# Kernel optimization log

Hardware: AMD Instinct MI355X
Metric: run time of the kernel (lower is better)

## Reference

```python
import jax, jax.numpy as jnp
import numpy as np

D_MODEL = 1024
NUM_HEADS = 16
SEQ_LEN = 2048
BATCH = 2
THETA = 10000.0


def apply_rope(x, positions, theta=THETA):
    # x: [b, h, s, d]; positions: [s] int
    d = x.shape[-1]
    inv_freq = 1.0 / (theta ** (jnp.arange(0, d, 2, dtype=jnp.float32) / d))  # [d/2]
    ang = positions.astype(jnp.float32)[:, None] * inv_freq[None, :]  # [s, d/2]
    cos, sin = jnp.cos(ang), jnp.sin(ang)  # [s, d/2]
    x_even = x[..., 0::2]
    x_odd = x[..., 1::2]
    out_even = x_even * cos - x_odd * sin
    out_odd = x_even * sin + x_odd * cos
    # re-interleave pairs
    out = jnp.stack([out_even, out_odd], axis=-1).reshape(x.shape)
    return out


def setup_inputs() -> dict:
    key = jax.random.key(0)
    ks = jax.random.split(key, 5)
    scale = 1.0 / np.sqrt(D_MODEL)
    return {
        "in_features": jax.random.normal(ks[0], (BATCH, SEQ_LEN, D_MODEL), dtype=jnp.float32),
        "token_positions": jnp.arange(SEQ_LEN, dtype=jnp.int32),
        "q_w": jax.random.normal(ks[1], (D_MODEL, D_MODEL), dtype=jnp.float32) * scale,
        "k_w": jax.random.normal(ks[2], (D_MODEL, D_MODEL), dtype=jnp.float32) * scale,
        "v_w": jax.random.normal(ks[3], (D_MODEL, D_MODEL), dtype=jnp.float32) * scale,
        "o_w": jax.random.normal(ks[4], (D_MODEL, D_MODEL), dtype=jnp.float32) * scale,
    }


def reference(in_features, token_positions, q_w, k_w, v_w, o_w):
    b, s, _ = in_features.shape
    h = NUM_HEADS
    d_k = D_MODEL // h

    # Linear stores weights [out, in]: y = x @ W^T
    def proj(x, w):
        y = jnp.einsum('bsi,oi->bso', x, w)
        return y.reshape(b, s, h, d_k).transpose(0, 2, 1, 3)  # [b, h, s, d]

    q = apply_rope(proj(in_features, q_w), token_positions)
    k = apply_rope(proj(in_features, k_w), token_positions)
    v = proj(in_features, v_w)

    scores = jnp.einsum('bhqd,bhkd->bhqk', q, k) / jnp.sqrt(jnp.float32(d_k))
    causal = jnp.tril(jnp.ones((s, s), dtype=bool))
    scores = jnp.where(causal, scores, jnp.float32(-1e30))
    attn = jax.nn.softmax(scores, axis=-1)
    out = jnp.einsum('bhqk,bhkd->bhqd', attn, v)  # [b, h, s, d]
    out = out.transpose(0, 2, 1, 3).reshape(b, s, h * d_k)
    return jnp.einsum('bsi,oi->bso', out, o_w)
```

## Files before the change

### kernel.cpp

```cpp
#include <hip/hip_runtime.h>
#include <hip/hip_bf16.h>

typedef unsigned short ushort_t;
typedef unsigned int uint_t;
typedef __attribute__((ext_vector_type(4))) float f32x4;
typedef __attribute__((ext_vector_type(16))) float f32x16;
typedef __attribute__((ext_vector_type(8))) short short8;
typedef __attribute__((ext_vector_type(4))) short short4x;
typedef __attribute__((ext_vector_type(4))) unsigned short u16x4;
typedef __attribute__((ext_vector_type(2))) uint_t u32x2;

typedef const __attribute__((address_space(1))) unsigned char glob_t;
typedef __attribute__((address_space(3))) unsigned char lds_t;

#define S_LEN 2048
#define DM 1024
#define NH 16
#define DH 64
#define NB 2
#define BH (NB*NH)
#define MROWS (NB*S_LEN)

#define SCALE_L2E 0.18033688f

__device__ __forceinline__ float bf2f(ushort_t u) {
    return __uint_as_float(((uint_t)u) << 16);
}
__device__ __forceinline__ ushort_t f2bf(float f) {
    __hip_bfloat16 h = __float2bfloat16(f);
    return *reinterpret_cast<ushort_t*>(&h);
}

__global__ __launch_bounds__(256) void convert_all(
    const float* __restrict__ X,  const float* __restrict__ Wq,
    const float* __restrict__ Wk, const float* __restrict__ Wv,
    const float* __restrict__ Wo,
    ushort_t* __restrict__ Xb,  ushort_t* __restrict__ Wqb,
    ushort_t* __restrict__ Wkb, ushort_t* __restrict__ Wvb,
    ushort_t* __restrict__ Wob)
{
    size_t i = (size_t)blockIdx.x * 256 + threadIdx.x;
    size_t e = i * 4;
    const float* src; ushort_t* dst; size_t off;
    if (e < (size_t)MROWS * DM) { src = X; dst = Xb; off = e; }
    else {
        size_t r = e - (size_t)MROWS * DM;
        int w = (int)(r >> 20); off = r & 1048575;
        src = (w == 0) ? Wq : (w == 1) ? Wk : (w == 2) ? Wv : Wo;
        dst = (w == 0) ? Wqb : (w == 1) ? Wkb : (w == 2) ? Wvb : Wob;
    }
    float4 v = *reinterpret_cast<const float4*>(src + off);
    u16x4 o;
    o[0] = f2bf(v.x); o[1] = f2bf(v.y); o[2] = f2bf(v.z); o[3] = f2bf(v.w);
    *reinterpret_cast<u16x4*>(dst + off) = o;
}

__global__ __launch_bounds__(256) void rope_table_k(
    const int* __restrict__ pos, float2* __restrict__ tab)
{
    int i = blockIdx.x * 256 + threadIdx.x;
    int s = i >> 5, f = i & 31;
    float inv = powf(10000.0f, -(float)f / 32.0f);
    float ang = (float)pos[s] * inv;
    tab[i] = make_float2(cosf(ang), sinf(ang));
}

template<int MODE>
__global__ __launch_bounds__(256) void gemm128b(
    const ushort_t* __restrict__ A,
    const ushort_t* __restrict__ W0, const ushort_t* __restrict__ W1,
    const ushort_t* __restrict__ W2,
    ushort_t* __restrict__ D0, ushort_t* __restrict__ D1,
    ushort_t* __restrict__ D2,
    float* __restrict__ Fout, const float2* __restrict__ tab)
{
    __shared__ __attribute__((aligned(16))) ushort_t As[128 * 32];
    __shared__ __attribute__((aligned(16))) ushort_t Bs[128 * 32];
    const ushort_t* W = (MODE == 1 || blockIdx.z == 0) ? W0
                        : (blockIdx.z == 1 ? W1 : W2);
    ushort_t* Dst = (blockIdx.z == 0) ? D0 : (blockIdx.z == 1) ? D1 : D2;
    int m0 = blockIdx.x * 128, n0 = blockIdx.y * 128;
    int tid = threadIdx.x, lane = tid & 63, wv = tid >> 6;
    int wm = wv >> 1, wn = wv & 1;
    int l15 = lane & 15, g = lane >> 4;

    f32x4 acc[4][4];
    for (int i = 0; i < 4; i++)
        for (int j = 0; j < 4; j++)
            acc[i][j] = (f32x4){0.f, 0.f, 0.f, 0.f};

    int srow = wv * 32 + (lane >> 2);
    int scol = (lane & 3) * 8;
    const ushort_t* Ap = A + (size_t)(m0 + srow) * DM + scol;
    const ushort_t* Wp = W + (size_t)(n0 + srow) * DM + scol;
    lds_t* laA0 = (lds_t*)&As[wv * 1024];
    lds_t* laA1 = (lds_t*)&As[wv * 1024 + 512];
    lds_t* laB0 = (lds_t*)&Bs[wv * 1024];
    lds_t* laB1 = (lds_t*)&Bs[wv * 1024 + 512];

    for (int kk = 0; kk < DM; kk += 32) {
        __builtin_amdgcn_global_load_lds((glob_t*)(Ap + kk), laA0, 16, 0, 0);
        __builtin_amdgcn_global_load_lds((glob_t*)(Ap + 16 * DM + kk), laA1, 16, 0, 0);
        __builtin_amdgcn_global_load_lds((glob_t*)(Wp + kk), laB0, 16, 0, 0);
        __builtin_amdgcn_global_load_lds((glob_t*)(Wp + 16 * DM + kk), laB1, 16, 0, 0);
        __syncthreads();
        short8 af[4], bf[4];
        for (int i = 0; i < 4; i++)
            af[i] = *reinterpret_cast<const short8*>(
                &As[(wm * 64 + i * 16 + l15) * 32 + g * 8]);
        for (int j = 0; j < 4; j++)
            bf[j] = *reinterpret_cast<const short8*>(
                &Bs[(wn * 64 + j * 16 + l15) * 32 + g * 8]);
        __builtin_amdgcn_s_setprio(1);
        for (int i = 0; i < 4; i++)
            for (int j = 0; j < 4; j++)
                acc[i][j] = __builtin_amdgcn_mfma_f32_16x16x32_bf16(
                    af[i], bf[j], acc[i][j], 0, 0, 0);
        __builtin_amdgcn_s_setprio(0);
        __syncthreads();
    }

    for (int i = 0; i < 4; i++) {
        for (int j = 0; j < 4; j++) {
            int mbase = m0 + wm * 64 + i * 16 + g * 4;
            int n = n0 + wn * 64 + j * 16 + l15;
            if (MODE == 0) {
                int h = n >> 6, d = n & 63;
                if (blockIdx.z < 2) {
                    int f = d >> 1;
                    float sgn = (d & 1) ? 1.f : -1.f;
                    float sc = (blockIdx.z == 0) ? SCALE_L2E : 1.0f;
                    for (int r = 0; r < 4; r++) {
                        int m = mbase + r;
                        int b = m >> 11, s = m & 2047;
                        float v = acc[i][j][r];
                        float p = __shfl_xor(v, 1);
                        float2 cs = tab[s * 32 + f];
                        float out = (v * cs.x + p * cs.y * sgn) * sc;
                        Dst[(((size_t)(b * NH + h)) * S_LEN + s) * DH + d] =
                            f2bf(out);
                    }
                } else {
                    for (int r = 0; r < 4; r++) {
                        int m = mbase + r;
                        int b = m >> 11, s = m & 2047;
                        Dst[((size_t)(b * NH + h) * DH + d) * S_LEN + s] =
                            f2bf(acc[i][j][r]);
                    }
                }
            } else {
                for (int r = 0; r < 4; r++)
                    Fout[(size_t)(mbase + r) * DM + n] = acc[i][j][r];
            }
        }
    }
}

#define WAITV4 asm volatile("s_waitcnt vmcnt(4)" ::: "memory")
#define WAITV0 asm volatile("s_waitcnt vmcnt(0)" ::: "memory")

__global__ __launch_bounds__(256, 2) void attn_k8(
    const ushort_t* __restrict__ Q, const ushort_t* __restrict__ K,
    const ushort_t* __restrict__ Vt, ushort_t* __restrict__ O)
{
    __shared__ __attribute__((aligned(16))) ushort_t Ks[3][4096];
    __shared__ __attribute__((aligned(16))) ushort_t Vs[3][4096];

    int tid = threadIdx.x, wv = tid >> 6, lane = tid & 63;
    int l31 = lane & 31, h = lane >> 5, r7 = l31 & 7;
    int bid = blockIdx.x;
    int grp = bid >> 5;
    int u = (bid < 256) ? (15 - grp) : (grp - 8);
    int bh = bid & 31;
    int qb0 = u * 128;
    int qmin = qb0 + wv * 32, qmax = qmin + 31;
    int nt = 2 * u + 2;

    const ushort_t* Qp = Q + (size_t)bh * S_LEN * DH;
    const char* Kp = (const char*)(K + (size_t)bh * S_LEN * DH);
    const char* Vp = (const char*)(Vt + (size_t)bh * DH * S_LEN);

    short8 qf[4];
    {
        const ushort_t* qp = Qp + (((size_t)(qmin + l31)) << 6) + h * 8;
        #pragma unroll
        for (int ds = 0; ds < 4; ds++)
            qf[ds] = *reinterpret_cast<const short8*>(qp + ds * 16);
    }

    f32x16 oacc[2];
    oacc[0] = (f32x16){0.f};
    oacc[1] = (f32x16){0.f};
    float m_run = -INFINITY, l_run = 0.f;

#define STAGE8(buf, kk0) do {                                                 \
    _Pragma("unroll") for (int c_ = 0; c_ < 2; ++c_) {                        \
        int L_ = c_ * 4096 + wv * 1024 + lane * 16;                           \
        int row_ = L_ >> 7;                                                   \
        int col_ = (L_ & 127) ^ ((row_ & 7) << 4);                            \
        __builtin_amdgcn_global_load_lds(                                     \
            (glob_t*)(Kp + (size_t)((kk0) + row_) * 128 + col_),              \
            (lds_t*)((char*)&Ks[buf][0] + c_ * 4096 + wv * 1024), 16, 0, 0);  \
        __builtin_amdgcn_global_load_lds(                                     \
            (glob_t*)(Vp + (size_t)row_ * (S_LEN * 2) + (size_t)(kk0) * 2     \
                      + col_),                                                \
            (lds_t*)((char*)&Vs[buf][0] + c_ * 4096 + wv * 1024), 16, 0, 0);  \
    } } while (0)

    STAGE8(0, 0);
    STAGE8(1, 64);
    WAITV4;
    __builtin_amdgcn_s_barrier();

    int cs = 0;
    for (int t = 0; t < nt; ++t) {
        int k0 = t << 6;
        int s2 = (cs >= 1) ? cs - 1 : cs + 2;
        bool willstage = (t + 2 < nt);
        if (willstage) STAGE8(s2, (t + 2) << 6);

        if (k0 <= qmax) {
            const char* kb = (const char*)&Ks[cs][0];
            const char* vbp = (const char*)&Vs[cs][0];
            short8 kf[2][4];
            #pragma unroll
            for (int s = 0; s < 2; s++)
                #pragma unroll
                for (int ds = 0; ds < 4; ds++)
                    kf[s][ds] = *reinterpret_cast<const short8*>(
                        kb + (s * 32 + l31) * 128 + (((h + 2 * ds) ^ r7) << 4));
            short4x vb[2][2][4];
            #pragma unroll
            for (int ss = 0; ss < 2; ss++)
                #pragma unroll
                for (int db = 0; db < 2; db++)
                    #pragma unroll
                    for (int kt = 0; kt < 4; kt++)
                        vb[ss][db][kt] = *reinterpret_cast<const short4x*>(
                            vbp + (db * 32 + l31) * 128
                            + ((((ss << 2) + kt) ^ r7) << 4) + h * 8);

            f32x16 st[2];
            __builtin_amdgcn_s_setprio(1);
            #pragma unroll
            for (int s = 0; s < 2; s++) {
                f32x16 z = {0.f};
                #pragma unroll
                for (int ds = 0; ds < 4; ds++)
                    z = __builtin_amdgcn_mfma_f32_32x32x16_bf16(
                        kf[s][ds], qf[ds], z, 0, 0, 0);
                st[s] = z;
            }
            __builtin_amdgcn_s_setprio(0);

            if (k0 + 63 > qmin) {
                int q = qmin + l31;
                #pragma unroll
                for (int s = 0; s < 2; s++)
                    #pragma unroll
                    for (int r = 0; r < 16; r++)
                        if ((k0 + s * 32 + (r & 3) + 8 * (r >> 2) + 4 * h) > q)
                            st[s][r] = -1e30f;
            }

            float m0v = st[0][0], m1v = st[1][0];
            #pragma unroll
            for (int r = 1; r < 15; r += 2) {
                m0v = fmaxf(fmaxf(m0v, st[0][r]), st[0][r + 1]);
                m1v = fmaxf(fmaxf(m1v, st[1][r]), st[1][r + 1]);
            }
            m0v = fmaxf(m0v, st[0][15]);
            m1v = fmaxf(m1v, st[1][15]);
            float m16 = fmaxf(m0v, m1v);
            m16 = fmaxf(m16, __shfl_xor(m16, 32));

            if (!__all(m16 <= m_run + 11.5f)) {
                float m_new = fmaxf(m_run, m16);
                float alpha = exp2f(m_run - m_new);
                m_run = m_new;
                l_run *= alpha;
                oacc[0] *= alpha;
                oacc[1] *= alpha;
            }

            float ps = 0.f;
            short4x pa[2][4];
            #pragma unroll
            for (int s = 0; s < 2; s++)
                #pragma unroll
                for (int kt = 0; kt < 4; kt++) {
                    float p0 = exp2f(st[s][4 * kt + 0] - m_run);
                    float p1 = exp2f(st[s][4 * kt + 1] - m_run);
                    float p2 = exp2f(st[s][4 * kt + 2] - m_run);
                    float p3 = exp2f(st[s][4 * kt + 3] - m_run);
                    ps += (p0 + p1) + (p2 + p3);
                    u32x2 w = { (uint_t)f2bf(p0) | ((uint_t)f2bf(p1) << 16),
                                (uint_t)f2bf(p2) | ((uint_t)f2bf(p3) << 16) };
                    pa[s][kt] = __builtin_bit_cast(short4x, w);
                }
            ps += __shfl_xor(ps, 32);
            l_run += ps;

            __builtin_amdgcn_s_setprio(1);
            #pragma unroll
            for (int s = 0; s < 2; s++)
                #pragma unroll
                for (int kt = 0; kt < 4; kt++) {
                    oacc[0] = __builtin_amdgcn_mfma_f32_32x32x8bf16_1k(
                        vb[s][0][kt], pa[s][kt], oacc[0], 0, 0, 0);
                    oacc[1] = __builtin_amdgcn_mfma_f32_32x32x8bf16_1k(
                        vb[s][1][kt], pa[s][kt], oacc[1], 0, 0, 0);
                }
            __builtin_amdgcn_s_setprio(0);
        }

        if (willstage) { WAITV4; } else { WAITV0; }
        __builtin_amdgcn_s_barrier();
        cs = (cs >= 2) ? 0 : cs + 1;
    }

    float inv = 1.0f / l_run;
    int b = bh >> 4, head = bh & 15;
    int q_row = qmin + l31;
    size_t obase = ((size_t)b * S_LEN + q_row) * DM + head * DH;
    #pragma unroll
    for (int db = 0; db < 2; db++)
        #pragma unroll
        for (int rg = 0; rg < 4; rg++) {
            u16x4 o;
            #pragma unroll
            for (int j = 0; j < 4; j++)
                o[j] = f2bf(oacc[db][rg * 4 + j] * inv);
            *reinterpret_cast<u16x4*>(&O[obase + db * 32 + rg * 8 + h * 4]) = o;
        }
#undef STAGE8
}

extern "C" void kernel_launch(void* const* d_in, const int* in_sizes, int n_in,
                              void* d_out, int out_size, void* d_ws, size_t ws_size,
                              hipStream_t stream)
{
    const float* X  = (const float*)d_in[0];
    const int* pos  = (const int*)d_in[1];
    const float* qw = (const float*)d_in[2];
    const float* kw = (const float*)d_in[3];
    const float* vw = (const float*)d_in[4];
    const float* ow = (const float*)d_in[5];
    float* out = (float*)d_out;

    char* ws = (char*)d_ws;
    ushort_t* Xb   = (ushort_t*)(ws);
    ushort_t* Wqb  = (ushort_t*)(ws + 8388608);
    ushort_t* Wkb  = (ushort_t*)(ws + 10485760);
    ushort_t* Wvb  = (ushort_t*)(ws + 12582912);
    ushort_t* Wob  = (ushort_t*)(ws + 14680064);
    ushort_t* Qbh  = (ushort_t*)(ws + 16777216);
    ushort_t* Kbh  = (ushort_t*)(ws + 25165824);
    ushort_t* Vtb  = (ushort_t*)(ws + 41943040);
    ushort_t* AttO = (ushort_t*)(ws + 50331648);
    float2*   tab  = (float2*)(ws + 58720256);

    convert_all<<<8192, 256, 0, stream>>>(X, qw, kw, vw, ow,
                                          Xb, Wqb, Wkb, Wvb, Wob);
    rope_table_k<<<256, 256, 0, stream>>>(pos, tab);
    gemm128b<0><<<dim3(32, 8, 3), 256, 0, stream>>>(
        Xb, Wqb, Wkb, Wvb, Qbh, Kbh, Vtb, nullptr, tab);
    attn_k8<<<512, 256, 0, stream>>>(Qbh, Kbh, Vtb, AttO);
    gemm128b<1><<<dim3(32, 8, 1), 256, 0, stream>>>(
        AttO, Wob, nullptr, nullptr, nullptr, nullptr, nullptr, out, tab);
}
```

Before: 145.1 us.

## Pair mirrored causal query blocks in one 512-thread attention workgroup sharing K/V tiles

```diff
diff --git a/kernel.cpp b/kernel.cpp
--- a/kernel.cpp
+++ b/kernel.cpp
@@ -156,10 +156,10 @@
     }
 }
 
-#define WAITV4 asm volatile("s_waitcnt vmcnt(4)" ::: "memory")
+#define WAITV2 asm volatile("s_waitcnt vmcnt(2)" ::: "memory")
 #define WAITV0 asm volatile("s_waitcnt vmcnt(0)" ::: "memory")
 
-__global__ __launch_bounds__(256, 2) void attn_k8(
+__global__ __launch_bounds__(512, 1) void attn_k9(
     const ushort_t* __restrict__ Q, const ushort_t* __restrict__ K,
     const ushort_t* __restrict__ Vt, ushort_t* __restrict__ O)
 {
@@ -169,12 +169,12 @@
     int tid = threadIdx.x, wv = tid >> 6, lane = tid & 63;
     int l31 = lane & 31, h = lane >> 5, r7 = l31 & 7;
     int bid = blockIdx.x;
-    int grp = bid >> 5;
-    int u = (bid < 256) ? (15 - grp) : (grp - 8);
+    int p = bid >> 5;
     int bh = bid & 31;
-    int qb0 = u * 128;
-    int qmin = qb0 + wv * 32, qmax = qmin + 31;
-    int nt = 2 * u + 2;
+    int uB = 15 - p;
+    int myu = (wv < 4) ? uB : p;
+    int qmin = myu * 128 + (wv & 3) * 32, qmax = qmin + 31;
+    int nt = 2 * uB + 2;
 
     const ushort_t* Qp = Q + (size_t)bh * S_LEN * DH;
     const char* Kp = (const char*)(K + (size_t)bh * S_LEN * DH);
@@ -193,23 +193,22 @@
     oacc[1] = (f32x16){0.f};
     float m_run = -INFINITY, l_run = 0.f;
 
-#define STAGE8(buf, kk0) do {                                                 \
-    _Pragma("unroll") for (int c_ = 0; c_ < 2; ++c_) {                        \
-        int L_ = c_ * 4096 + wv * 1024 + lane * 16;                           \
+#define STAGE9(buf, kk0) do {                                                 \
+        int L_ = tid * 16;                                                    \
         int row_ = L_ >> 7;                                                   \
         int col_ = (L_ & 127) ^ ((row_ & 7) << 4);                            \
         __builtin_amdgcn_global_load_lds(                                     \
             (glob_t*)(Kp + (size_t)((kk0) + row_) * 128 + col_),              \
-            (lds_t*)((char*)&Ks[buf][0] + c_ * 4096 + wv * 1024), 16, 0, 0);  \
+            (lds_t*)((char*)&Ks[buf][0] + wv * 1024), 16, 0, 0);              \
         __builtin_amdgcn_global_load_lds(                                     \
             (glob_t*)(Vp + (size_t)row_ * (S_LEN * 2) + (size_t)(kk0) * 2     \
                       + col_),                                                \
-            (lds_t*)((char*)&Vs[buf][0] + c_ * 4096 + wv * 1024), 16, 0, 0);  \
-    } } while (0)
-
-    STAGE8(0, 0);
-    STAGE8(1, 64);
-    WAITV4;
+            (lds_t*)((char*)&Vs[buf][0] + wv * 1024), 16, 0, 0);              \
+    } while (0)
+
+    STAGE9(0, 0);
+    STAGE9(1, 64);
+    WAITV2;
     __builtin_amdgcn_s_barrier();
 
     int cs = 0;
@@ -217,7 +216,7 @@
         int k0 = t << 6;
         int s2 = (cs >= 1) ? cs - 1 : cs + 2;
         bool willstage = (t + 2 < nt);
-        if (willstage) STAGE8(s2, (t + 2) << 6);
+        if (willstage) STAGE9(s2, (t + 2) << 6);
 
         if (k0 <= qmax) {
             const char* kb = (const char*)&Ks[cs][0];
@@ -314,7 +313,7 @@
             __builtin_amdgcn_s_setprio(0);
         }
 
-        if (willstage) { WAITV4; } else { WAITV0; }
+        if (willstage) { WAITV2; } else { WAITV0; }
         __builtin_amdgcn_s_barrier();
         cs = (cs >= 2) ? 0 : cs + 1;
     }
@@ -333,7 +332,7 @@
                 o[j] = f2bf(oacc[db][rg * 4 + j] * inv);
             *reinterpret_cast<u16x4*>(&O[obase + db * 32 + rg * 8 + h * 4]) = o;
         }
-#undef STAGE8
+#undef STAGE9
 }
 
 extern "C" void kernel_launch(void* const* d_in, const int* in_sizes, int n_in,
@@ -365,7 +364,7 @@
     rope_table_k<<<256, 256, 0, stream>>>(pos, tab);
     gemm128b<0><<<dim3(32, 8, 3), 256, 0, stream>>>(
         Xb, Wqb, Wkb, Wvb, Qbh, Kbh, Vtb, nullptr, tab);
-    attn_k8<<<512, 256, 0, stream>>>(Qbh, Kbh, Vtb, AttO);
+    attn_k9<<<256, 512, 0, stream>>>(Qbh, Kbh, Vtb, AttO);
     gemm128b<1><<<dim3(32, 8, 1), 256, 0, stream>>>(
         AttO, Wob, nullptr, nullptr, nullptr, nullptr, nullptr, out, tab);
 }
```

Result: no change. 146.8 us (+1.2%).

## Pair causal query tiles per 512-thread block with 128-key shared K/V tiles

Applied to the files above, without the earlier changes.

```diff
diff --git a/kernel.cpp b/kernel.cpp
--- a/kernel.cpp
+++ b/kernel.cpp
@@ -159,22 +159,22 @@
 #define WAITV4 asm volatile("s_waitcnt vmcnt(4)" ::: "memory")
 #define WAITV0 asm volatile("s_waitcnt vmcnt(0)" ::: "memory")
 
-__global__ __launch_bounds__(256, 2) void attn_k8(
+__global__ __launch_bounds__(512, 1) void attn_k10(
     const ushort_t* __restrict__ Q, const ushort_t* __restrict__ K,
     const ushort_t* __restrict__ Vt, ushort_t* __restrict__ O)
 {
-    __shared__ __attribute__((aligned(16))) ushort_t Ks[3][4096];
-    __shared__ __attribute__((aligned(16))) ushort_t Vs[3][4096];
+    __shared__ __attribute__((aligned(16))) ushort_t Ks[3][8192];
+    __shared__ __attribute__((aligned(16))) ushort_t Vs[3][8192];
 
     int tid = threadIdx.x, wv = tid >> 6, lane = tid & 63;
     int l31 = lane & 31, h = lane >> 5, r7 = l31 & 7;
     int bid = blockIdx.x;
-    int grp = bid >> 5;
-    int u = (bid < 256) ? (15 - grp) : (grp - 8);
+    int p = bid >> 5;
     int bh = bid & 31;
-    int qb0 = u * 128;
-    int qmin = qb0 + wv * 32, qmax = qmin + 31;
-    int nt = 2 * u + 2;
+    int uB = 15 - p;
+    int myu = (wv < 4) ? uB : p;
+    int qmin = myu * 128 + (wv & 3) * 32, qmax = qmin + 31;
+    int ntr = uB + 1;
 
     const ushort_t* Qp = Q + (size_t)bh * S_LEN * DH;
     const char* Kp = (const char*)(K + (size_t)bh * S_LEN * DH);
@@ -193,85 +193,82 @@
     oacc[1] = (f32x16){0.f};
     float m_run = -INFINITY, l_run = 0.f;
 
-#define STAGE8(buf, kk0) do {                                                 \
+#define STAGE10(buf, kk0) do {                                                \
     _Pragma("unroll") for (int c_ = 0; c_ < 2; ++c_) {                        \
-        int L_ = c_ * 4096 + wv * 1024 + lane * 16;                           \
-        int row_ = L_ >> 7;                                                   \
-        int col_ = (L_ & 127) ^ ((row_ & 7) << 4);                            \
+        int Lk_ = c_ * 8192 + tid * 16;                                       \
+        int rk_ = Lk_ >> 7;                                                   \
+        int ck_ = (Lk_ & 127) ^ ((rk_ & 7) << 4);                             \
         __builtin_amdgcn_global_load_lds(                                     \
-            (glob_t*)(Kp + (size_t)((kk0) + row_) * 128 + col_),              \
-            (lds_t*)((char*)&Ks[buf][0] + c_ * 4096 + wv * 1024), 16, 0, 0);  \
+            (glob_t*)(Kp + (size_t)((kk0) + rk_) * 128 + ck_),                \
+            (lds_t*)((char*)&Ks[buf][0] + c_ * 8192 + wv * 1024), 16, 0, 0);  \
+        int rv_ = Lk_ >> 8;                                                   \
+        int cb_ = Lk_ & 255;                                                  \
+        int cv_ = ((cb_ & 127) ^ ((rv_ & 7) << 4)) | (cb_ & 128);             \
         __builtin_amdgcn_global_load_lds(                                     \
-            (glob_t*)(Vp + (size_t)row_ * (S_LEN * 2) + (size_t)(kk0) * 2     \
-                      + col_),                                                \
-            (lds_t*)((char*)&Vs[buf][0] + c_ * 4096 + wv * 1024), 16, 0, 0);  \
+            (glob_t*)(Vp + (size_t)rv_ * (S_LEN * 2) + (size_t)(kk0) * 2      \
+                      + cv_),                                                 \
+            (lds_t*)((char*)&Vs[buf][0] + c_ * 8192 + wv * 1024), 16, 0, 0);  \
     } } while (0)
 
-    STAGE8(0, 0);
-    STAGE8(1, 64);
+    STAGE10(0, 0);
+    STAGE10(1, 128);
     WAITV4;
     __builtin_amdgcn_s_barrier();
 
     int cs = 0;
-    for (int t = 0; t < nt; ++t) {
-        int k0 = t << 6;
+    for (int t = 0; t < ntr; ++t) {
+        int k0 = t << 7;
         int s2 = (cs >= 1) ? cs - 1 : cs + 2;
-        bool willstage = (t + 2 < nt);
-        if (willstage) STAGE8(s2, (t + 2) << 6);
+        bool willstage = (t + 2 < ntr);
+        if (willstage) STAGE10(s2, (t + 2) << 7);
 
         if (k0 <= qmax) {
             const char* kb = (const char*)&Ks[cs][0];
             const char* vbp = (const char*)&Vs[cs][0];
-            short8 kf[2][4];
-            #pragma unroll
-            for (int s = 0; s < 2; s++)
+
+            f32x16 st[4];
+            #pragma unroll
+            for (int s = 0; s < 4; s++) {
+                short8 kf[4];
                 #pragma unroll
                 for (int ds = 0; ds < 4; ds++)
-                    kf[s][ds] = *reinterpret_cast<const short8*>(
+                    kf[ds] = *reinterpret_cast<const short8*>(
                         kb + (s * 32 + l31) * 128 + (((h + 2 * ds) ^ r7) << 4));
-            short4x vb[2][2][4];
-            #pragma unroll
-            for (int ss = 0; ss < 2; ss++)
-                #pragma unroll
-                for (int db = 0; db < 2; db++)
-                    #pragma unroll
-                    for (int kt = 0; kt < 4; kt++)
-                        vb[ss][db][kt] = *reinterpret_cast<const short4x*>(
-                            vbp + (db * 32 + l31) * 128
-                            + ((((ss << 2) + kt) ^ r7) << 4) + h * 8);
-
-            f32x16 st[2];
-            __builtin_amdgcn_s_setprio(1);
-            #pragma unroll
-            for (int s = 0; s < 2; s++) {
+                __builtin_amdgcn_s_setprio(1);
                 f32x16 z = {0.f};
                 #pragma unroll
                 for (int ds = 0; ds < 4; ds++)
                     z = __builtin_amdgcn_mfma_f32_32x32x16_bf16(
-                        kf[s][ds], qf[ds], z, 0, 0, 0);
+                        kf[ds], qf[ds], z, 0, 0, 0);
                 st[s] = z;
-            }
-            __builtin_amdgcn_s_setprio(0);
-
-            if (k0 + 63 > qmin) {
+                __builtin_amdgcn_s_setprio(0);
+            }
+
+            if (k0 + 127 > qmin) {
                 int q = qmin + l31;
                 #pragma unroll
-                for (int s = 0; s < 2; s++)
+                for (int s = 0; s < 4; s++)
                     #pragma unroll
                     for (int r = 0; r < 16; r++)
                         if ((k0 + s * 32 + (r & 3) + 8 * (r >> 2) + 4 * h) > q)
                             st[s][r] = -1e30f;
             }
 
-            float m0v = st[0][0], m1v = st[1][0];
-            #pragma unroll
-            for (int r = 1; r < 15; r += 2) {
-                m0v = fmaxf(fmaxf(m0v, st[0][r]), st[0][r + 1]);
-                m1v = fmaxf(fmaxf(m1v, st[1][r]), st[1][r + 1]);
-            }
-            m0v = fmaxf(m0v, st[0][15]);
-            m1v = fmaxf(m1v, st[1][15]);
-            float m16 = fmaxf(m0v, m1v);
+            float mv[4];
+            #pragma unroll
+            for (int s = 0; s < 4; s++) {
+                float a0 = fmaxf(st[s][0], st[s][1]);
+                float a1 = fmaxf(st[s][2], st[s][3]);
+                float a2 = fmaxf(st[s][4], st[s][5]);
+                float a3 = fmaxf(st[s][6], st[s][7]);
+                float a4 = fmaxf(st[s][8], st[s][9]);
+                float a5 = fmaxf(st[s][10], st[s][11]);
+                float a6 = fmaxf(st[s][12], st[s][13]);
+                float a7 = fmaxf(st[s][14], st[s][15]);
+                mv[s] = fmaxf(fmaxf(fmaxf(a0, a1), fmaxf(a2, a3)),
+                              fmaxf(fmaxf(a4, a5), fmaxf(a6, a7)));
+            }
+            float m16 = fmaxf(fmaxf(mv[0], mv[1]), fmaxf(mv[2], mv[3]));
             m16 = fmaxf(m16, __shfl_xor(m16, 32));
 
             if (!__all(m16 <= m_run + 11.5f)) {
@@ -284,9 +281,9 @@
             }
 
             float ps = 0.f;
-            short4x pa[2][4];
-            #pragma unroll
-            for (int s = 0; s < 2; s++)
+            short4x pa[4][4];
+            #pragma unroll
+            for (int s = 0; s < 4; s++)
                 #pragma unroll
                 for (int kt = 0; kt < 4; kt++) {
                     float p0 = exp2f(st[s][4 * kt + 0] - m_run);
@@ -301,17 +298,29 @@
             ps += __shfl_xor(ps, 32);
             l_run += ps;
 
-            __builtin_amdgcn_s_setprio(1);
-            #pragma unroll
-            for (int s = 0; s < 2; s++)
+            #pragma unroll
+            for (int s = 0; s < 4; s++) {
+                short4x vb[2][4];
+                #pragma unroll
+                for (int db = 0; db < 2; db++)
+                    #pragma unroll
+                    for (int kt = 0; kt < 4; kt++) {
+                        int c = s * 4 + kt;
+                        vb[db][kt] = *reinterpret_cast<const short4x*>(
+                            vbp + (db * 32 + l31) * 256
+                            + ((((c & 7) ^ r7) << 4) | ((c >> 3) << 7))
+                            + h * 8);
+                    }
+                __builtin_amdgcn_s_setprio(1);
                 #pragma unroll
                 for (int kt = 0; kt < 4; kt++) {
                     oacc[0] = __builtin_amdgcn_mfma_f32_32x32x8bf16_1k(
-                        vb[s][0][kt], pa[s][kt], oacc[0], 0, 0, 0);
+                        vb[0][kt], pa[s][kt], oacc[0], 0, 0, 0);
                     oacc[1] = __builtin_amdgcn_mfma_f32_32x32x8bf16_1k(
-                        vb[s][1][kt], pa[s][kt], oacc[1], 0, 0, 0);
+                        vb[1][kt], pa[s][kt], oacc[1], 0, 0, 0);
                 }
-            __builtin_amdgcn_s_setprio(0);
+                __builtin_amdgcn_s_setprio(0);
+            }
         }
 
         if (willstage) { WAITV4; } else { WAITV0; }
@@ -333,7 +342,7 @@
                 o[j] = f2bf(oacc[db][rg * 4 + j] * inv);
             *reinterpret_cast<u16x4*>(&O[obase + db * 32 + rg * 8 + h * 4]) = o;
         }
-#undef STAGE8
+#undef STAGE10
 }
 
 extern "C" void kernel_launch(void* const* d_in, const int* in_sizes, int n_in,
@@ -365,7 +374,7 @@
     rope_table_k<<<256, 256, 0, stream>>>(pos, tab);
     gemm128b<0><<<dim3(32, 8, 3), 256, 0, stream>>>(
         Xb, Wqb, Wkb, Wvb, Qbh, Kbh, Vtb, nullptr, tab);
-    attn_k8<<<512, 256, 0, stream>>>(Qbh, Kbh, Vtb, AttO);
+    attn_k10<<<256, 512, 0, stream>>>(Qbh, Kbh, Vtb, AttO);
     gemm128b<1><<<dim3(32, 8, 1), 256, 0, stream>>>(
         AttO, Wob, nullptr, nullptr, nullptr, nullptr, nullptr, out, tab);
 }
```

New measurement: 132.5 us. -8.7%, faster.
